# Performance work log

Measured on AMD Instinct MI355X. Metric: run time of the kernel, lower is better.

## Reference

```python
import jax, jax.numpy as jnp
import numpy as np

N = 16384
D = 128

def setup_inputs() -> dict:
    key = jax.random.key(0)
    k1, k2 = jax.random.split(key)
    point_cloud1 = jax.random.normal(k1, (1, N, D), dtype=jnp.float32)
    point_cloud2 = jax.random.normal(k2, (1, N, D), dtype=jnp.float32)
    return {"point_cloud1": point_cloud1, "point_cloud2": point_cloud2}

def reference(point_cloud1, point_cloud2):
    # Squared pairwise distances via the expansion ||a-b||^2 = ||a||^2 + ||b||^2 - 2 a.b
    # (mathematically identical to the original broadcast-subtract form, but avoids
    #  materializing the [1, N, N, D] intermediate).
    a2 = jnp.sum(point_cloud1 * point_cloud1, axis=-1)          # [1, N]
    b2 = jnp.sum(point_cloud2 * point_cloud2, axis=-1)          # [1, N]
    ab = jnp.einsum('bnd,bmd->bnm', point_cloud1, point_cloud2) # [1, N, N]
    dists_squared = a2[:, :, None] + b2[:, None, :] - 2.0 * ab  # [1, N, N]
    min_dists1 = jnp.min(dists_squared, axis=2)  # nearest in cloud2 for each point in cloud1
    min_dists2 = jnp.min(dists_squared, axis=1)  # nearest in cloud1 for each point in cloud2
    return jnp.mean(min_dists1) + jnp.mean(min_dists2)
```

## Files before the change

### kernel.cpp

```cpp
#include <hip/hip_runtime.h>
#include <hip/hip_bf16.h>

#define N_PTS 16384
#define DIM   128
#define KAUG  144
#define ROWB  (KAUG * 2)
#define NCHUNK 18

typedef __bf16 bf16x8 __attribute__((ext_vector_type(8)));
typedef float  f32x4  __attribute__((ext_vector_type(4)));
typedef float  f32x16 __attribute__((ext_vector_type(16)));

__device__ __forceinline__ unsigned fmap(float f) {
    unsigned u = __float_as_uint(f);
    return (u & 0x80000000u) ? ~u : (u | 0x80000000u);
}
__device__ __forceinline__ float funmap(unsigned u) {
    return __uint_as_float((u & 0x80000000u) ? (u & 0x7FFFFFFFu) : ~u);
}

__device__ __forceinline__ void gload_lds16(const void* g, void* l) {
    __builtin_amdgcn_global_load_lds(
        (const __attribute__((address_space(1))) void*)g,
        (__attribute__((address_space(3))) void*)l, 16, 0, 0);
}

__global__ void chamfer_prep5(const float* __restrict__ A, const float* __restrict__ B,
                              unsigned short* __restrict__ Ax, unsigned short* __restrict__ Bx,
                              unsigned* __restrict__ minbuf) {
    int gtid = blockIdx.x * 256 + threadIdx.x;
    if (gtid < 4 * N_PTS) minbuf[gtid] = 0xFFFFFFFFu;

    int wave = blockIdx.x * 4 + (threadIdx.x >> 6);
    int lane = threadIdx.x & 63;
    int isB  = wave >= N_PTS;
    int row  = isB ? (wave - N_PTS) : wave;
    const float* src = isB ? B : A;
    unsigned short* dst = isB ? Bx : Ax;

    float2 v = *reinterpret_cast<const float2*>(&src[(size_t)row * DIM + lane * 2]);

    float sc = isB ? 1.f : -2.f;
    __bf16 bx = (__bf16)(sc * v.x), by = (__bf16)(sc * v.y);
    ushort2 st;
    st.x = __builtin_bit_cast(unsigned short, bx);
    st.y = __builtin_bit_cast(unsigned short, by);
    *reinterpret_cast<ushort2*>(&dst[(size_t)row * KAUG + lane * 2]) = st;

    float s = fmaf(v.x, v.x, v.y * v.y);
    #pragma unroll
    for (int off = 1; off < 64; off <<= 1) s += __shfl_xor(s, off);

    __bf16 hb = (__bf16)s;
    float  hf = (float)hb;
    __bf16 lb = (__bf16)(s - hf);
    unsigned short hu = __builtin_bit_cast(unsigned short, hb);
    unsigned short lu = __builtin_bit_cast(unsigned short, lb);
    const unsigned short one = 0x3F80;

    if (lane < 8) {
        ushort2 tw; tw.x = 0; tw.y = 0;
        if (lane == 0) { tw.x = isB ? hu : one; tw.y = isB ? lu : one; }
        if (lane == 1) { tw.x = isB ? one : hu; tw.y = isB ? one : lu; }
        *reinterpret_cast<ushort2*>(&dst[(size_t)row * KAUG + 128 + lane * 2]) = tw;
    }
}

__global__ __launch_bounds__(256, 2)
void chamfer_gemm_min5(const unsigned short* __restrict__ Ax,
                       const unsigned short* __restrict__ Bx,
                       unsigned* __restrict__ rowminS,
                       unsigned* __restrict__ colminS) {
    __shared__ __align__(16) unsigned char sB[2][36864];

    const int b   = blockIdx.x;
    const int tm  = (b >> 2) * 128;
    const int tn0 = (b & 3) * 32;

    const int t = threadIdx.x, w = t >> 6, lane = t & 63;
    const int ll = lane & 31, hi = lane >> 5;
    const int wr = (w >> 1) * 64, wc = (w & 1) * 64;

    bf16x8 af[2][9];
    #pragma unroll
    for (int mi = 0; mi < 2; ++mi) {
        const unsigned short* ap = Ax + (size_t)(tm + wr + mi * 32 + ll) * KAUG + hi * 8;
        #pragma unroll
        for (int ks = 0; ks < 9; ++ks)
            af[mi][ks] = *reinterpret_cast<const bf16x8*>(ap + ks * 16);
    }

    int goff[9];
    #pragma unroll
    for (int j = 0; j < 9; ++j) {
        int chunk = j * 256 + t;
        int r = chunk / NCHUNK;
        int s = chunk - r * NCHUNK;
        int c = (s < 16) ? (s ^ (r & 7)) : (16 + ((s - 16) ^ (r & 1)));
        goff[j] = r * KAUG + c * 8;
    }

    {
        const unsigned short* bp = Bx + (size_t)tn0 * 128 * KAUG;
        #pragma unroll
        for (int j = 0; j < 9; ++j)
            gload_lds16(bp + goff[j], sB[0] + (j * 256 + t) * 16);
    }
    __syncthreads();

    float rmin_part[32];
    #pragma unroll
    for (int k = 0; k < 32; ++k) rmin_part[k] = 3.4e38f;

    const int rA = wc + ll;
    const int rB = wc + 32 + ll;

    for (int it = 0; it < 32; ++it) {
        const int cur = it & 1;
        const int tn  = tn0 + it;

        if (it + 1 < 32) {
            const unsigned short* bp = Bx + (size_t)(tn + 1) * 128 * KAUG;
            #pragma unroll
            for (int j = 0; j < 9; ++j)
                gload_lds16(bp + goff[j], sB[cur ^ 1] + (j * 256 + t) * 16);
        }

        f32x16 acc[2][2] = {};
        #pragma unroll
        for (int ks = 0; ks < 9; ++ks) {
            const int c = ks * 2 + hi;
            const int sA0 = (c < 16) ? (c ^ (rA & 7)) : (16 + ((c - 16) ^ (rA & 1)));
            const int sB1 = (c < 16) ? (c ^ (rB & 7)) : (16 + ((c - 16) ^ (rB & 1)));
            bf16x8 b0 = *reinterpret_cast<const bf16x8*>(&sB[cur][rA * ROWB + sA0 * 16]);
            bf16x8 b1 = *reinterpret_cast<const bf16x8*>(&sB[cur][rB * ROWB + sB1 * 16]);
            #pragma unroll
            for (int mi = 0; mi < 2; ++mi) {
                acc[mi][0] = __builtin_amdgcn_mfma_f32_32x32x16_bf16(af[mi][ks], b0, acc[mi][0], 0, 0, 0);
                acc[mi][1] = __builtin_amdgcn_mfma_f32_32x32x16_bf16(af[mi][ks], b1, acc[mi][1], 0, 0, 0);
            }
        }

        #pragma unroll
        for (int mi = 0; mi < 2; ++mi)
            #pragma unroll
            for (int reg = 0; reg < 16; ++reg)
                rmin_part[mi * 16 + reg] =
                    fminf(rmin_part[mi * 16 + reg], fminf(acc[mi][0][reg], acc[mi][1][reg]));

        float cm0 = acc[0][0][0], cm1 = acc[0][1][0];
        #pragma unroll
        for (int mi = 0; mi < 2; ++mi)
            #pragma unroll
            for (int reg = 0; reg < 16; ++reg) {
                if (mi | reg) {
                    cm0 = fminf(cm0, acc[mi][0][reg]);
                    cm1 = fminf(cm1, acc[mi][1][reg]);
                }
            }
        cm0 = fminf(cm0, __shfl_xor(cm0, 32));
        cm1 = fminf(cm1, __shfl_xor(cm1, 32));
        float cmSel = hi ? cm1 : cm0;
        const int own_col = tn * 128 + wc + hi * 32 + ll;

        __syncthreads();

        atomicMin(&colminS[(size_t)(w >> 1) * N_PTS + own_col], fmap(cmSel));
    }

    #pragma unroll
    for (int s = 16; s >= 1; s >>= 1) {
        #pragma unroll
        for (int k = 0; k < 16; ++k) {
            if (k < s) {
                float snd = (ll & s) ? rmin_part[k] : rmin_part[k + s];
                float r = __shfl_xor(snd, s);
                rmin_part[k] = (ll & s) ? fminf(rmin_part[k + s], r) : fminf(rmin_part[k], r);
            }
        }
    }
    const int own_row = tm + wr + ((ll >> 4) << 5) + (ll & 3) + (((ll >> 2) & 3) << 3) + (hi << 2);
    atomicMin(&rowminS[(size_t)(w & 1) * N_PTS + own_row], fmap(rmin_part[0]));
}

__global__ void chamfer_finalize4(const unsigned* __restrict__ rowminS,
                                  const unsigned* __restrict__ colminS,
                                  float* __restrict__ out) {
    __shared__ double sred[16];
    int t = threadIdx.x;
    double s = 0.0;
    for (int i = t; i < N_PTS; i += 1024) {
        unsigned rm = min(rowminS[i], rowminS[i + N_PTS]);
        unsigned cm = min(colminS[i], colminS[i + N_PTS]);
        s += (double)funmap(rm) + (double)funmap(cm);
    }
    #pragma unroll
    for (int off = 32; off; off >>= 1) s += __shfl_down(s, off);
    if ((t & 63) == 0) sred[t >> 6] = s;
    __syncthreads();
    if (t == 0) {
        double tot = 0.0;
        #pragma unroll
        for (int i = 0; i < 16; ++i) tot += sred[i];
        out[0] = (float)(tot * (1.0 / (double)N_PTS));
    }
}

__global__ void chamfer_prep2(const float* __restrict__ A, const float* __restrict__ B,
                              unsigned short* __restrict__ Abf, unsigned short* __restrict__ Bbf,
                              float* __restrict__ a2, float* __restrict__ b2,
                              unsigned* __restrict__ rowmin, unsigned* __restrict__ colmin) {
    int wave = blockIdx.x * 4 + (threadIdx.x >> 6);
    int lane = threadIdx.x & 63;
    int isB  = wave >= N_PTS;
    int row  = isB ? (wave - N_PTS) : wave;
    const float* src = isB ? B : A;
    unsigned short* dst = isB ? Bbf : Abf;

    float2 v = *reinterpret_cast<const float2*>(&src[(size_t)row * DIM + lane * 2]);
    __bf16 bx = (__bf16)v.x, by = (__bf16)v.y;
    ushort2 st;
    st.x = __builtin_bit_cast(unsigned short, bx);
    st.y = __builtin_bit_cast(unsigned short, by);
    *reinterpret_cast<ushort2*>(&dst[(size_t)row * DIM + lane * 2]) = st;

    float s = fmaf(v.x, v.x, v.y * v.y);
    #pragma unroll
    for (int off = 32; off; off >>= 1) s += __shfl_down(s, off);
    if (lane == 0) {
        if (isB) { b2[row] = s; colmin[row] = 0xFFFFFFFFu; }
        else     { a2[row] = s; rowmin[row] = 0xFFFFFFFFu; }
    }
}

__global__ __launch_bounds__(512, 2)
void chamfer_gemm_min3(const unsigned short* __restrict__ Abf, const unsigned short* __restrict__ Bbf,
                       const float* __restrict__ a2, const float* __restrict__ b2,
                       unsigned* __restrict__ rowmin, unsigned* __restrict__ colmin) {
    __shared__ __align__(16) unsigned char sA[65536];
    __shared__ __align__(16) unsigned char sB2[2][32768];

    const int b = blockIdx.x;
    const int tm_base = (b >> 2) * 256;
    const int tn0 = (b & 3) * 32;

    const int t = threadIdx.x;
    const int w = t >> 6, lane = t & 63;
    const int lq = lane >> 4, lr = lane & 15;
    const int wr = (w >> 1) * 64;
    const int wc = (w & 1) * 64;

    #pragma unroll
    for (int j = 0; j < 8; ++j) {
        int chunk = ((w << 3) + j) * 64 + lane;
        int r = chunk >> 4, kc = (chunk & 15) ^ (r & 7);
        gload_lds16(Abf + (size_t)(tm_base + r) * DIM + kc * 8, sA + chunk * 16);
    }
    #pragma unroll
    for (int j = 0; j < 4; ++j) {
        int chunk = ((w << 2) + j) * 64 + lane;
        int r = chunk >> 4, kc = (chunk & 15) ^ (r & 7);
        gload_lds16(Bbf + (size_t)(tn0 * 128 + r) * DIM + kc * 8, sB2[0] + chunk * 16);
    }

    float a2v[4][4];
    #pragma unroll
    for (int mi = 0; mi < 4; ++mi) {
        float4 q = *reinterpret_cast<const float4*>(&a2[tm_base + wr + mi * 16 + lq * 4]);
        a2v[mi][0] = q.x; a2v[mi][1] = q.y; a2v[mi][2] = q.z; a2v[mi][3] = q.w;
    }
    __syncthreads();

    for (int it = 0; it < 32; ++it) {
        const int cur = it & 1;
        const int tn = tn0 + it;

        if (it + 1 < 32) {
            #pragma unroll
            for (int j = 0; j < 4; ++j) {
                int chunk = ((w << 2) + j) * 64 + lane;
                int r = chunk >> 4, kc = (chunk & 15) ^ (r & 7);
                gload_lds16(Bbf + (size_t)((tn + 1) * 128 + r) * DIM + kc * 8,
                            sB2[cur ^ 1] + chunk * 16);
            }
        }

        f32x4 acc[4][4] = {};
        #pragma unroll
        for (int ks = 0; ks < 4; ++ks) {
            const int kc = ks * 4 + lq;
            bf16x8 af2[4], bfr[4];
            #pragma unroll
            for (int mi = 0; mi < 4; ++mi) {
                int r = wr + mi * 16 + lr;
                af2[mi] = *reinterpret_cast<const bf16x8*>(&sA[r * 256 + ((kc * 16) ^ ((r & 7) << 4))]);
            }
            #pragma unroll
            for (int ni = 0; ni < 4; ++ni) {
                int r = wc + ni * 16 + lr;
                bfr[ni] = *reinterpret_cast<const bf16x8*>(&sB2[cur][r * 256 + ((kc * 16) ^ ((r & 7) << 4))]);
            }
            #pragma unroll
            for (int mi = 0; mi < 4; ++mi)
                #pragma unroll
                for (int ni = 0; ni < 4; ++ni)
                    acc[mi][ni] = __builtin_amdgcn_mfma_f32_16x16x32_bf16(af2[mi], bfr[ni], acc[mi][ni], 0, 0, 0);
        }

        const int col_base = tn * 128 + wc;
        float b2v[4];
        #pragma unroll
        for (int ni = 0; ni < 4; ++ni) b2v[ni] = b2[col_base + ni * 16 + lr];

        float v[16];
        #pragma unroll
        for (int mi = 0; mi < 4; ++mi) {
            #pragma unroll
            for (int j = 0; j < 4; ++j) {
                float m = fmaf(-2.f, acc[mi][0][j], b2v[0]);
                m = fminf(m, fmaf(-2.f, acc[mi][1][j], b2v[1]));
                m = fminf(m, fmaf(-2.f, acc[mi][2][j], b2v[2]));
                m = fminf(m, fmaf(-2.f, acc[mi][3][j], b2v[3]));
                v[mi * 4 + j] = m;
            }
        }
        #pragma unroll
        for (int k = 0; k < 8; ++k) {
            float s = (lr & 8) ? v[k] : v[k + 8];
            float r = __shfl_xor(s, 8);
            v[k] = (lr & 8) ? fminf(v[k + 8], r) : fminf(v[k], r);
        }
        #pragma unroll
        for (int k = 0; k < 4; ++k) {
            float s = (lr & 4) ? v[k] : v[k + 4];
            float r = __shfl_xor(s, 4);
            v[k] = (lr & 4) ? fminf(v[k + 4], r) : fminf(v[k], r);
        }
        #pragma unroll
        for (int k = 0; k < 2; ++k) {
            float s = (lr & 2) ? v[k] : v[k + 2];
            float r = __shfl_xor(s, 2);
            v[k] = (lr & 2) ? fminf(v[k + 2], r) : fminf(v[k], r);
        }
        {
            float s = (lr & 1) ? v[0] : v[1];
            float r = __shfl_xor(s, 1);
            v[0] = (lr & 1) ? fminf(v[1], r) : fminf(v[0], r);
        }
        const int own_row = tm_base + wr + ((lr >> 2) << 4) + (lq << 2) + (lr & 3);

        float cp[4];
        #pragma unroll
        for (int ni = 0; ni < 4; ++ni) {
            float m = fmaf(-2.f, acc[0][ni][0], a2v[0][0]);
            #pragma unroll
            for (int mi = 0; mi < 4; ++mi)
                #pragma unroll
                for (int j = 0; j < 4; ++j)
                    if (mi | j) m = fminf(m, fmaf(-2.f, acc[mi][ni][j], a2v[mi][j]));
            cp[ni] = m;
        }
        #pragma unroll
        for (int k = 0; k < 2; ++k) {
            float s = (lane & 16) ? cp[k] : cp[k + 2];
            float r = __shfl_xor(s, 16);
            cp[k] = (lane & 16) ? fminf(cp[k + 2], r) : fminf(cp[k], r);
        }
        float cfin;
        {
            float s = (lane & 32) ? cp[0] : cp[1];
            float r = __shfl_xor(s, 32);
            cfin = (lane & 32) ? fminf(cp[1], r) : fminf(cp[0], r);
        }
        const int ni_own = ((lq & 1) << 1) | (lq >> 1);
        const int own_col = col_base + ni_own * 16 + lr;

        __syncthreads();

        atomicMin(&rowmin[own_row], fmap(v[0]));
        atomicMin(&colmin[own_col], fmap(cfin));
    }
}

__global__ void chamfer_finalize2(const unsigned* __restrict__ rowmin,
                                  const unsigned* __restrict__ colmin,
                                  const float* __restrict__ a2, const float* __restrict__ b2,
                                  float* __restrict__ out) {
    __shared__ double sred[16];
    int t = threadIdx.x;
    double s = 0.0;
    for (int i = t; i < N_PTS; i += 1024)
        s += ((double)funmap(rowmin[i]) + (double)a2[i])
           + ((double)funmap(colmin[i]) + (double)b2[i]);
    #pragma unroll
    for (int off = 32; off; off >>= 1) s += __shfl_down(s, off);
    if ((t & 63) == 0) sred[t >> 6] = s;
    __syncthreads();
    if (t == 0) {
        double tot = 0.0;
        #pragma unroll
        for (int i = 0; i < 16; ++i) tot += sred[i];
        out[0] = (float)(tot * (1.0 / (double)N_PTS));
    }
}

extern "C" void kernel_launch(void* const* d_in, const int* in_sizes, int n_in,
                              void* d_out, int out_size, void* d_ws, size_t ws_size,
                              hipStream_t stream) {
    const float* A = (const float*)d_in[0];
    const float* B = (const float*)d_in[1];
    float* out = (float*)d_out;
    char* ws = (char*)d_ws;

    const size_t SZ5   = (size_t)N_PTS * KAUG * sizeof(unsigned short);
    const size_t need5 = 2 * SZ5 + 4 * (size_t)N_PTS * 4;

    const size_t BF    = (size_t)N_PTS * DIM * sizeof(unsigned short);
    const size_t need3 = 2 * BF + 4 * (size_t)(1 << 16);

    if (ws_size >= need5) {
        unsigned short* Ax = (unsigned short*)(ws);
        unsigned short* Bx = (unsigned short*)(ws + SZ5);
        unsigned* minbuf   = (unsigned*)(ws + 2 * SZ5);
        unsigned* rowminS  = minbuf;
        unsigned* colminS  = minbuf + 2 * N_PTS;

        chamfer_prep5<<<(2 * N_PTS) / 4, 256, 0, stream>>>(A, B, Ax, Bx, minbuf);
        chamfer_gemm_min5<<<512, 256, 0, stream>>>(Ax, Bx, rowminS, colminS);
        chamfer_finalize4<<<1, 1024, 0, stream>>>(rowminS, colminS, out);
    } else if (ws_size >= need3) {
        unsigned short* Abf = (unsigned short*)(ws);
        unsigned short* Bbf = (unsigned short*)(ws + BF);
        float*    a2     = (float*)(ws + 2 * BF);
        float*    b2     = (float*)(ws + 2 * BF + (1 << 16));
        unsigned* rowmin = (unsigned*)(ws + 2 * BF + (2 << 16));
        unsigned* colmin = (unsigned*)(ws + 2 * BF + (3 << 16));

        chamfer_prep2<<<(2 * N_PTS) / 4, 256, 0, stream>>>(A, B, Abf, Bbf, a2, b2, rowmin, colmin);
        chamfer_gemm_min3<<<256, 512, 0, stream>>>(Abf, Bbf, a2, b2, rowmin, colmin);
        chamfer_finalize2<<<1, 1024, 0, stream>>>(rowmin, colmin, a2, b2, out);
    }
}
```

Baseline: 102.1 us.

## Drop LDS staging; stream transposed B fragments directly from global per wave

The prep kernel now writes B in a fragment-major transposed layout, so each lane's 16-byte MFMA operand sits contiguously for coalesced direct global loads. The GEMM becomes single-wave blocks (2048 blocks of 64 threads), each covering 64 rows by 2048 columns, with no shared memory, no double buffering and no barriers. Column minima are now spread over four partial buffers and merged in finalize. This removes the LDS traffic and sync overhead, but every wave re-reads B from global/L2 without any reuse across waves and has no explicit prefetch, so the kernel may become latency- or bandwidth-bound.

```diff
diff --git a/kernel.cpp b/kernel.cpp
--- a/kernel.cpp
+++ b/kernel.cpp
@@ -4,7 +4,6 @@
 #define N_PTS 16384
 #define DIM   128
 #define KAUG  144
-#define ROWB  (KAUG * 2)
 #define NCHUNK 18
 
 typedef __bf16 bf16x8 __attribute__((ext_vector_type(8)));
@@ -25,18 +24,17 @@
         (__attribute__((address_space(3))) void*)l, 16, 0, 0);
 }
 
-__global__ void chamfer_prep5(const float* __restrict__ A, const float* __restrict__ B,
-                              unsigned short* __restrict__ Ax, unsigned short* __restrict__ Bx,
+__global__ void chamfer_prep6(const float* __restrict__ A, const float* __restrict__ B,
+                              unsigned short* __restrict__ Ax, unsigned short* __restrict__ BxT,
                               unsigned* __restrict__ minbuf) {
     int gtid = blockIdx.x * 256 + threadIdx.x;
-    if (gtid < 4 * N_PTS) minbuf[gtid] = 0xFFFFFFFFu;
+    if (gtid < 6 * N_PTS) minbuf[gtid] = 0xFFFFFFFFu;
 
     int wave = blockIdx.x * 4 + (threadIdx.x >> 6);
     int lane = threadIdx.x & 63;
     int isB  = wave >= N_PTS;
     int row  = isB ? (wave - N_PTS) : wave;
     const float* src = isB ? B : A;
-    unsigned short* dst = isB ? Bx : Ax;
 
     float2 v = *reinterpret_cast<const float2*>(&src[(size_t)row * DIM + lane * 2]);
 
@@ -45,7 +43,6 @@
     ushort2 st;
     st.x = __builtin_bit_cast(unsigned short, bx);
     st.y = __builtin_bit_cast(unsigned short, by);
-    *reinterpret_cast<ushort2*>(&dst[(size_t)row * KAUG + lane * 2]) = st;
 
     float s = fmaf(v.x, v.x, v.y * v.y);
     #pragma unroll
@@ -58,87 +55,68 @@
     unsigned short lu = __builtin_bit_cast(unsigned short, lb);
     const unsigned short one = 0x3F80;
 
-    if (lane < 8) {
-        ushort2 tw; tw.x = 0; tw.y = 0;
-        if (lane == 0) { tw.x = isB ? hu : one; tw.y = isB ? lu : one; }
-        if (lane == 1) { tw.x = isB ? one : hu; tw.y = isB ? one : lu; }
-        *reinterpret_cast<ushort2*>(&dst[(size_t)row * KAUG + 128 + lane * 2]) = tw;
-    }
-}
-
-__global__ __launch_bounds__(256, 2)
-void chamfer_gemm_min5(const unsigned short* __restrict__ Ax,
-                       const unsigned short* __restrict__ Bx,
+    ushort2 tw; tw.x = 0; tw.y = 0;
+    if (lane == 0) { tw.x = isB ? hu : one; tw.y = isB ? lu : one; }
+    if (lane == 1) { tw.x = isB ? one : hu; tw.y = isB ? one : lu; }
+
+    if (!isB) {
+        *reinterpret_cast<ushort2*>(&Ax[(size_t)row * KAUG + lane * 2]) = st;
+        if (lane < 8)
+            *reinterpret_cast<ushort2*>(&Ax[(size_t)row * KAUG + 128 + lane * 2]) = tw;
+    } else {
+        unsigned pd = (unsigned)st.x | ((unsigned)st.y << 16);
+        *reinterpret_cast<unsigned*>((char*)BxT +
+            ((size_t)(lane >> 2) * N_PTS + row) * 16 + (lane & 3) * 4) = pd;
+        if (lane < 8) {
+            unsigned pa = (unsigned)tw.x | ((unsigned)tw.y << 16);
+            *reinterpret_cast<unsigned*>((char*)BxT +
+                ((size_t)(16 + (lane >> 2)) * N_PTS + row) * 16 + (lane & 3) * 4) = pa;
+        }
+    }
+}
+
+__global__ __launch_bounds__(64, 2)
+void chamfer_gemm_min6(const unsigned short* __restrict__ Ax,
+                       const unsigned short* __restrict__ BxT,
                        unsigned* __restrict__ rowminS,
                        unsigned* __restrict__ colminS) {
-    __shared__ __align__(16) unsigned char sB[2][36864];
-
-    const int b   = blockIdx.x;
-    const int tm  = (b >> 2) * 128;
-    const int tn0 = (b & 3) * 32;
-
-    const int t = threadIdx.x, w = t >> 6, lane = t & 63;
+    const int j  = blockIdx.x;
+    const int e  = j & 7;
+    const int mb = j >> 3;
+    const int tm = mb * 64;
+    const int col0 = e * 2048;
+
+    const int lane = threadIdx.x;
     const int ll = lane & 31, hi = lane >> 5;
-    const int wr = (w >> 1) * 64, wc = (w & 1) * 64;
 
     bf16x8 af[2][9];
     #pragma unroll
     for (int mi = 0; mi < 2; ++mi) {
-        const unsigned short* ap = Ax + (size_t)(tm + wr + mi * 32 + ll) * KAUG + hi * 8;
+        const unsigned short* ap = Ax + (size_t)(tm + mi * 32 + ll) * KAUG + hi * 8;
         #pragma unroll
         for (int ks = 0; ks < 9; ++ks)
             af[mi][ks] = *reinterpret_cast<const bf16x8*>(ap + ks * 16);
     }
 
-    int goff[9];
-    #pragma unroll
-    for (int j = 0; j < 9; ++j) {
-        int chunk = j * 256 + t;
-        int r = chunk / NCHUNK;
-        int s = chunk - r * NCHUNK;
-        int c = (s < 16) ? (s ^ (r & 7)) : (16 + ((s - 16) ^ (r & 1)));
-        goff[j] = r * KAUG + c * 8;
-    }
-
-    {
-        const unsigned short* bp = Bx + (size_t)tn0 * 128 * KAUG;
-        #pragma unroll
-        for (int j = 0; j < 9; ++j)
-            gload_lds16(bp + goff[j], sB[0] + (j * 256 + t) * 16);
-    }
-    __syncthreads();
-
     float rmin_part[32];
     #pragma unroll
     for (int k = 0; k < 32; ++k) rmin_part[k] = 3.4e38f;
 
-    const int rA = wc + ll;
-    const int rB = wc + 32 + ll;
+    const char* bbase = (const char*)BxT + ((size_t)hi * N_PTS + col0 + ll) * 16;
+    const size_t KSTEP = (size_t)2 * N_PTS * 16;
 
     for (int it = 0; it < 32; ++it) {
-        const int cur = it & 1;
-        const int tn  = tn0 + it;
-
-        if (it + 1 < 32) {
-            const unsigned short* bp = Bx + (size_t)(tn + 1) * 128 * KAUG;
-            #pragma unroll
-            for (int j = 0; j < 9; ++j)
-                gload_lds16(bp + goff[j], sB[cur ^ 1] + (j * 256 + t) * 16);
-        }
+        const char* bp = bbase + (size_t)it * (64 * 16);
 
         f32x16 acc[2][2] = {};
         #pragma unroll
         for (int ks = 0; ks < 9; ++ks) {
-            const int c = ks * 2 + hi;
-            const int sA0 = (c < 16) ? (c ^ (rA & 7)) : (16 + ((c - 16) ^ (rA & 1)));
-            const int sB1 = (c < 16) ? (c ^ (rB & 7)) : (16 + ((c - 16) ^ (rB & 1)));
-            bf16x8 b0 = *reinterpret_cast<const bf16x8*>(&sB[cur][rA * ROWB + sA0 * 16]);
-            bf16x8 b1 = *reinterpret_cast<const bf16x8*>(&sB[cur][rB * ROWB + sB1 * 16]);
-            #pragma unroll
-            for (int mi = 0; mi < 2; ++mi) {
-                acc[mi][0] = __builtin_amdgcn_mfma_f32_32x32x16_bf16(af[mi][ks], b0, acc[mi][0], 0, 0, 0);
-                acc[mi][1] = __builtin_amdgcn_mfma_f32_32x32x16_bf16(af[mi][ks], b1, acc[mi][1], 0, 0, 0);
-            }
+            bf16x8 b0 = *reinterpret_cast<const bf16x8*>(bp + (size_t)ks * KSTEP);
+            bf16x8 b1 = *reinterpret_cast<const bf16x8*>(bp + (size_t)ks * KSTEP + 32 * 16);
+            acc[0][0] = __builtin_amdgcn_mfma_f32_32x32x16_bf16(af[0][ks], b0, acc[0][0], 0, 0, 0);
+            acc[1][0] = __builtin_amdgcn_mfma_f32_32x32x16_bf16(af[1][ks], b0, acc[1][0], 0, 0, 0);
+            acc[0][1] = __builtin_amdgcn_mfma_f32_32x32x16_bf16(af[0][ks], b1, acc[0][1], 0, 0, 0);
+            acc[1][1] = __builtin_amdgcn_mfma_f32_32x32x16_bf16(af[1][ks], b1, acc[1][1], 0, 0, 0);
         }
 
         #pragma unroll
@@ -161,11 +139,9 @@
         cm0 = fminf(cm0, __shfl_xor(cm0, 32));
         cm1 = fminf(cm1, __shfl_xor(cm1, 32));
         float cmSel = hi ? cm1 : cm0;
-        const int own_col = tn * 128 + wc + hi * 32 + ll;
-
-        __syncthreads();
-
-        atomicMin(&colminS[(size_t)(w >> 1) * N_PTS + own_col], fmap(cmSel));
+        const int own_col = col0 + it * 64 + hi * 32 + ll;
+
+        atomicMin(&colminS[(size_t)(mb & 3) * N_PTS + own_col], fmap(cmSel));
     }
 
     #pragma unroll
@@ -179,11 +155,11 @@
             }
         }
     }
-    const int own_row = tm + wr + ((ll >> 4) << 5) + (ll & 3) + (((ll >> 2) & 3) << 3) + (hi << 2);
-    atomicMin(&rowminS[(size_t)(w & 1) * N_PTS + own_row], fmap(rmin_part[0]));
-}
-
-__global__ void chamfer_finalize4(const unsigned* __restrict__ rowminS,
+    const int own_row = tm + ((ll >> 4) << 5) + (ll & 3) + (((ll >> 2) & 3) << 3) + (hi << 2);
+    atomicMin(&rowminS[(size_t)(e & 1) * N_PTS + own_row], fmap(rmin_part[0]));
+}
+
+__global__ void chamfer_finalize6(const unsigned* __restrict__ rowminS,
                                   const unsigned* __restrict__ colminS,
                                   float* __restrict__ out) {
     __shared__ double sred[16];
@@ -191,7 +167,8 @@
     double s = 0.0;
     for (int i = t; i < N_PTS; i += 1024) {
         unsigned rm = min(rowminS[i], rowminS[i + N_PTS]);
-        unsigned cm = min(colminS[i], colminS[i + N_PTS]);
+        unsigned cm = min(min(colminS[i],              colminS[i + N_PTS]),
+                          min(colminS[i + 2 * N_PTS],  colminS[i + 3 * N_PTS]));
         s += (double)funmap(rm) + (double)funmap(cm);
     }
     #pragma unroll
@@ -251,14 +228,14 @@
     const int wc = (w & 1) * 64;
 
     #pragma unroll
-    for (int j = 0; j < 8; ++j) {
-        int chunk = ((w << 3) + j) * 64 + lane;
+    for (int jj = 0; jj < 8; ++jj) {
+        int chunk = ((w << 3) + jj) * 64 + lane;
         int r = chunk >> 4, kc = (chunk & 15) ^ (r & 7);
         gload_lds16(Abf + (size_t)(tm_base + r) * DIM + kc * 8, sA + chunk * 16);
     }
     #pragma unroll
-    for (int j = 0; j < 4; ++j) {
-        int chunk = ((w << 2) + j) * 64 + lane;
+    for (int jj = 0; jj < 4; ++jj) {
+        int chunk = ((w << 2) + jj) * 64 + lane;
         int r = chunk >> 4, kc = (chunk & 15) ^ (r & 7);
         gload_lds16(Bbf + (size_t)(tn0 * 128 + r) * DIM + kc * 8, sB2[0] + chunk * 16);
     }
@@ -277,8 +254,8 @@
 
         if (it + 1 < 32) {
             #pragma unroll
-            for (int j = 0; j < 4; ++j) {
-                int chunk = ((w << 2) + j) * 64 + lane;
+            for (int jj = 0; jj < 4; ++jj) {
+                int chunk = ((w << 2) + jj) * 64 + lane;
                 int r = chunk >> 4, kc = (chunk & 15) ^ (r & 7);
                 gload_lds16(Bbf + (size_t)((tn + 1) * 128 + r) * DIM + kc * 8,
                             sB2[cur ^ 1] + chunk * 16);
@@ -316,12 +293,12 @@
         #pragma unroll
         for (int mi = 0; mi < 4; ++mi) {
             #pragma unroll
-            for (int j = 0; j < 4; ++j) {
-                float m = fmaf(-2.f, acc[mi][0][j], b2v[0]);
-                m = fminf(m, fmaf(-2.f, acc[mi][1][j], b2v[1]));
-                m = fminf(m, fmaf(-2.f, acc[mi][2][j], b2v[2]));
-                m = fminf(m, fmaf(-2.f, acc[mi][3][j], b2v[3]));
-                v[mi * 4 + j] = m;
+            for (int jj = 0; jj < 4; ++jj) {
+                float m = fmaf(-2.f, acc[mi][0][jj], b2v[0]);
+                m = fminf(m, fmaf(-2.f, acc[mi][1][jj], b2v[1]));
+                m = fminf(m, fmaf(-2.f, acc[mi][2][jj], b2v[2]));
+                m = fminf(m, fmaf(-2.f, acc[mi][3][jj], b2v[3]));
+                v[mi * 4 + jj] = m;
             }
         }
         #pragma unroll
@@ -356,8 +333,8 @@
             #pragma unroll
             for (int mi = 0; mi < 4; ++mi)
                 #pragma unroll
-                for (int j = 0; j < 4; ++j)
-                    if (mi | j) m = fminf(m, fmaf(-2.f, acc[mi][ni][j], a2v[mi][j]));
+                for (int jj = 0; jj < 4; ++jj)
+                    if (mi | jj) m = fminf(m, fmaf(-2.f, acc[mi][ni][jj], a2v[mi][jj]));
             cp[ni] = m;
         }
         #pragma unroll
@@ -412,22 +389,22 @@
     float* out = (float*)d_out;
     char* ws = (char*)d_ws;
 
-    const size_t SZ5   = (size_t)N_PTS * KAUG * sizeof(unsigned short);
-    const size_t need5 = 2 * SZ5 + 4 * (size_t)N_PTS * 4;
+    const size_t SZ6   = (size_t)N_PTS * KAUG * sizeof(unsigned short);
+    const size_t need6 = 2 * SZ6 + 6 * (size_t)N_PTS * 4;
 
     const size_t BF    = (size_t)N_PTS * DIM * sizeof(unsigned short);
     const size_t need3 = 2 * BF + 4 * (size_t)(1 << 16);
 
-    if (ws_size >= need5) {
-        unsigned short* Ax = (unsigned short*)(ws);
-        unsigned short* Bx = (unsigned short*)(ws + SZ5);
-        unsigned* minbuf   = (unsigned*)(ws + 2 * SZ5);
-        unsigned* rowminS  = minbuf;
-        unsigned* colminS  = minbuf + 2 * N_PTS;
-
-        chamfer_prep5<<<(2 * N_PTS) / 4, 256, 0, stream>>>(A, B, Ax, Bx, minbuf);
-        chamfer_gemm_min5<<<512, 256, 0, stream>>>(Ax, Bx, rowminS, colminS);
-        chamfer_finalize4<<<1, 1024, 0, stream>>>(rowminS, colminS, out);
+    if (ws_size >= need6) {
+        unsigned short* Ax  = (unsigned short*)(ws);
+        unsigned short* BxT = (unsigned short*)(ws + SZ6);
+        unsigned* minbuf    = (unsigned*)(ws + 2 * SZ6);
+        unsigned* rowminS   = minbuf;
+        unsigned* colminS   = minbuf + 2 * N_PTS;
+
+        chamfer_prep6<<<(2 * N_PTS) / 4, 256, 0, stream>>>(A, B, Ax, BxT, minbuf);
+        chamfer_gemm_min6<<<2048, 64, 0, stream>>>(Ax, BxT, rowminS, colminS);
+        chamfer_finalize6<<<1, 1024, 0, stream>>>(rowminS, colminS, out);
     } else if (ws_size >= need3) {
         unsigned short* Abf = (unsigned short*)(ws);
         unsigned short* Bbf = (unsigned short*)(ws + BF);
```

Result: slower. 132.2 us (+29.5%).

## Deepen B-tile prefetch to two stages and split final reduction across blocks

Applied to the files above, without the earlier changes.

The GEMM-min kernel now preloads the first two B tiles and issues each next load two iterations ahead, after the MFMA phase. Full __syncthreads are replaced with explicit vmcnt waits plus raw s_barrier, and s_setprio raises wave priority around the MFMA loop. The single-block finalize is split into a 64-block partial-sum kernel and a tiny final kernel. This adds an extra launch and relies on exact hand-written vmcnt counts for correctness.

```diff
diff --git a/kernel.cpp b/kernel.cpp
--- a/kernel.cpp
+++ b/kernel.cpp
@@ -67,7 +67,7 @@
 }
 
 __global__ __launch_bounds__(256, 2)
-void chamfer_gemm_min5(const unsigned short* __restrict__ Ax,
+void chamfer_gemm_min7(const unsigned short* __restrict__ Ax,
                        const unsigned short* __restrict__ Bx,
                        unsigned* __restrict__ rowminS,
                        unsigned* __restrict__ colminS) {
@@ -101,12 +101,19 @@
     }
 
     {
-        const unsigned short* bp = Bx + (size_t)tn0 * 128 * KAUG;
+        const unsigned short* bp0 = Bx + (size_t)tn0 * 128 * KAUG;
+        const unsigned short* bp1 = Bx + (size_t)(tn0 + 1) * 128 * KAUG;
         #pragma unroll
         for (int j = 0; j < 9; ++j)
-            gload_lds16(bp + goff[j], sB[0] + (j * 256 + t) * 16);
-    }
-    __syncthreads();
+            gload_lds16(bp0 + goff[j], sB[0] + (j * 256 + t) * 16);
+        #pragma unroll
+        for (int j = 0; j < 9; ++j)
+            gload_lds16(bp1 + goff[j], sB[1] + (j * 256 + t) * 16);
+    }
+    asm volatile("s_waitcnt vmcnt(9)" ::: "memory");
+    __builtin_amdgcn_sched_barrier(0);
+    __builtin_amdgcn_s_barrier();
+    __builtin_amdgcn_sched_barrier(0);
 
     float rmin_part[32];
     #pragma unroll
@@ -119,13 +126,7 @@
         const int cur = it & 1;
         const int tn  = tn0 + it;
 
-        if (it + 1 < 32) {
-            const unsigned short* bp = Bx + (size_t)(tn + 1) * 128 * KAUG;
-            #pragma unroll
-            for (int j = 0; j < 9; ++j)
-                gload_lds16(bp + goff[j], sB[cur ^ 1] + (j * 256 + t) * 16);
-        }
-
+        __builtin_amdgcn_s_setprio(1);
         f32x16 acc[2][2] = {};
         #pragma unroll
         for (int ks = 0; ks < 9; ++ks) {
@@ -140,6 +141,18 @@
                 acc[mi][1] = __builtin_amdgcn_mfma_f32_32x32x16_bf16(af[mi][ks], b1, acc[mi][1], 0, 0, 0);
             }
         }
+        __builtin_amdgcn_s_setprio(0);
+
+        __builtin_amdgcn_sched_barrier(0);
+        __builtin_amdgcn_s_barrier();
+        __builtin_amdgcn_sched_barrier(0);
+
+        if (it + 2 < 32) {
+            const unsigned short* bp = Bx + (size_t)(tn + 2) * 128 * KAUG;
+            #pragma unroll
+            for (int j = 0; j < 9; ++j)
+                gload_lds16(bp + goff[j], sB[cur] + (j * 256 + t) * 16);
+        }
 
         #pragma unroll
         for (int mi = 0; mi < 2; ++mi)
@@ -163,7 +176,11 @@
         float cmSel = hi ? cm1 : cm0;
         const int own_col = tn * 128 + wc + hi * 32 + ll;
 
-        __syncthreads();
+        if (it < 30) { asm volatile("s_waitcnt vmcnt(9)" ::: "memory"); }
+        else         { asm volatile("s_waitcnt vmcnt(0)" ::: "memory"); }
+        __builtin_amdgcn_sched_barrier(0);
+        __builtin_amdgcn_s_barrier();
+        __builtin_amdgcn_sched_barrier(0);
 
         atomicMin(&colminS[(size_t)(w >> 1) * N_PTS + own_col], fmap(cmSel));
     }
@@ -183,27 +200,29 @@
     atomicMin(&rowminS[(size_t)(w & 1) * N_PTS + own_row], fmap(rmin_part[0]));
 }
 
-__global__ void chamfer_finalize4(const unsigned* __restrict__ rowminS,
-                                  const unsigned* __restrict__ colminS,
-                                  float* __restrict__ out) {
-    __shared__ double sred[16];
+__global__ void chamfer_partial7(const unsigned* __restrict__ rowminS,
+                                 const unsigned* __restrict__ colminS,
+                                 double* __restrict__ partials) {
+    __shared__ double sred[4];
     int t = threadIdx.x;
-    double s = 0.0;
-    for (int i = t; i < N_PTS; i += 1024) {
-        unsigned rm = min(rowminS[i], rowminS[i + N_PTS]);
-        unsigned cm = min(colminS[i], colminS[i + N_PTS]);
-        s += (double)funmap(rm) + (double)funmap(cm);
-    }
+    int i = blockIdx.x * 256 + t;
+    unsigned rm = min(rowminS[i], rowminS[i + N_PTS]);
+    unsigned cm = min(colminS[i], colminS[i + N_PTS]);
+    double s = (double)funmap(rm) + (double)funmap(cm);
     #pragma unroll
     for (int off = 32; off; off >>= 1) s += __shfl_down(s, off);
     if ((t & 63) == 0) sred[t >> 6] = s;
     __syncthreads();
-    if (t == 0) {
-        double tot = 0.0;
-        #pragma unroll
-        for (int i = 0; i < 16; ++i) tot += sred[i];
-        out[0] = (float)(tot * (1.0 / (double)N_PTS));
-    }
+    if (t == 0) partials[blockIdx.x] = sred[0] + sred[1] + sred[2] + sred[3];
+}
+
+__global__ void chamfer_final7(const double* __restrict__ partials,
+                               float* __restrict__ out) {
+    int t = threadIdx.x;
+    double s = partials[t];
+    #pragma unroll
+    for (int off = 32; off; off >>= 1) s += __shfl_down(s, off);
+    if (t == 0) out[0] = (float)(s * (1.0 / (double)N_PTS));
 }
 
 __global__ void chamfer_prep2(const float* __restrict__ A, const float* __restrict__ B,
@@ -251,14 +270,14 @@
     const int wc = (w & 1) * 64;
 
     #pragma unroll
-    for (int j = 0; j < 8; ++j) {
-        int chunk = ((w << 3) + j) * 64 + lane;
+    for (int jj = 0; jj < 8; ++jj) {
+        int chunk = ((w << 3) + jj) * 64 + lane;
         int r = chunk >> 4, kc = (chunk & 15) ^ (r & 7);
         gload_lds16(Abf + (size_t)(tm_base + r) * DIM + kc * 8, sA + chunk * 16);
     }
     #pragma unroll
-    for (int j = 0; j < 4; ++j) {
-        int chunk = ((w << 2) + j) * 64 + lane;
+    for (int jj = 0; jj < 4; ++jj) {
+        int chunk = ((w << 2) + jj) * 64 + lane;
         int r = chunk >> 4, kc = (chunk & 15) ^ (r & 7);
         gload_lds16(Bbf + (size_t)(tn0 * 128 + r) * DIM + kc * 8, sB2[0] + chunk * 16);
     }
@@ -277,8 +296,8 @@
 
         if (it + 1 < 32) {
             #pragma unroll
-            for (int j = 0; j < 4; ++j) {
-                int chunk = ((w << 2) + j) * 64 + lane;
+            for (int jj = 0; jj < 4; ++jj) {
+                int chunk = ((w << 2) + jj) * 64 + lane;
                 int r = chunk >> 4, kc = (chunk & 15) ^ (r & 7);
                 gload_lds16(Bbf + (size_t)((tn + 1) * 128 + r) * DIM + kc * 8,
                             sB2[cur ^ 1] + chunk * 16);
@@ -316,12 +335,12 @@
         #pragma unroll
         for (int mi = 0; mi < 4; ++mi) {
             #pragma unroll
-            for (int j = 0; j < 4; ++j) {
-                float m = fmaf(-2.f, acc[mi][0][j], b2v[0]);
-                m = fminf(m, fmaf(-2.f, acc[mi][1][j], b2v[1]));
-                m = fminf(m, fmaf(-2.f, acc[mi][2][j], b2v[2]));
-                m = fminf(m, fmaf(-2.f, acc[mi][3][j], b2v[3]));
-                v[mi * 4 + j] = m;
+            for (int jj = 0; jj < 4; ++jj) {
+                float m = fmaf(-2.f, acc[mi][0][jj], b2v[0]);
+                m = fminf(m, fmaf(-2.f, acc[mi][1][jj], b2v[1]));
+                m = fminf(m, fmaf(-2.f, acc[mi][2][jj], b2v[2]));
+                m = fminf(m, fmaf(-2.f, acc[mi][3][jj], b2v[3]));
+                v[mi * 4 + jj] = m;
             }
         }
         #pragma unroll
@@ -356,8 +375,8 @@
             #pragma unroll
             for (int mi = 0; mi < 4; ++mi)
                 #pragma unroll
-                for (int j = 0; j < 4; ++j)
-                    if (mi | j) m = fminf(m, fmaf(-2.f, acc[mi][ni][j], a2v[mi][j]));
+                for (int jj = 0; jj < 4; ++jj)
+                    if (mi | jj) m = fminf(m, fmaf(-2.f, acc[mi][ni][jj], a2v[mi][jj]));
             cp[ni] = m;
         }
         #pragma unroll
@@ -412,22 +431,24 @@
     float* out = (float*)d_out;
     char* ws = (char*)d_ws;
 
-    const size_t SZ5   = (size_t)N_PTS * KAUG * sizeof(unsigned short);
-    const size_t need5 = 2 * SZ5 + 4 * (size_t)N_PTS * 4;
+    const size_t SZ7   = (size_t)N_PTS * KAUG * sizeof(unsigned short);
+    const size_t need7 = 2 * SZ7 + 4 * (size_t)N_PTS * 4 + 64 * sizeof(double);
 
     const size_t BF    = (size_t)N_PTS * DIM * sizeof(unsigned short);
     const size_t need3 = 2 * BF + 4 * (size_t)(1 << 16);
 
-    if (ws_size >= need5) {
+    if (ws_size >= need7) {
         unsigned short* Ax = (unsigned short*)(ws);
-        unsigned short* Bx = (unsigned short*)(ws + SZ5);
-        unsigned* minbuf   = (unsigned*)(ws + 2 * SZ5);
+        unsigned short* Bx = (unsigned short*)(ws + SZ7);
+        unsigned* minbuf   = (unsigned*)(ws + 2 * SZ7);
         unsigned* rowminS  = minbuf;
         unsigned* colminS  = minbuf + 2 * N_PTS;
+        double*   partials = (double*)(ws + 2 * SZ7 + 4 * (size_t)N_PTS * 4);
 
         chamfer_prep5<<<(2 * N_PTS) / 4, 256, 0, stream>>>(A, B, Ax, Bx, minbuf);
-        chamfer_gemm_min5<<<512, 256, 0, stream>>>(Ax, Bx, rowminS, colminS);
-        chamfer_finalize4<<<1, 1024, 0, stream>>>(rowminS, colminS, out);
+        chamfer_gemm_min7<<<512, 256, 0, stream>>>(Ax, Bx, rowminS, colminS);
+        chamfer_partial7<<<64, 256, 0, stream>>>(rowminS, colminS, partials);
+        chamfer_final7<<<1, 64, 0, stream>>>(partials, out);
     } else if (ws_size >= need3) {
         unsigned short* Abf = (unsigned short*)(ws);
         unsigned short* Bbf = (unsigned short*)(ws + BF);
@@ -437,6 +458,7 @@
         unsigned* colmin = (unsigned*)(ws + 2 * BF + (3 << 16));
 
         chamfer_prep2<<<(2 * N_PTS) / 4, 256, 0, stream>>>(A, B, Abf, Bbf, a2, b2, rowmin, colmin);
+        dim3 grid(N_PTS / 128, N_PTS / 128);
         chamfer_gemm_min3<<<256, 512, 0, stream>>>(Abf, Bbf, a2, b2, rowmin, colmin);
         chamfer_finalize2<<<1, 1024, 0, stream>>>(rowmin, colmin, a2, b2, out);
     }
```

Result: faster. 99.55 us (median of 2 runs) (-2.5%).
